# Performance work log

Hardware: AMD Instinct MI355X
Metric: run time of the kernel (lower is better)

The kernel has to match this reference:

```python
import jax, jax.numpy as jnp
import numpy as np

T, B, D_IN, D_HID, D_OUT = 4096, 64, 64, 512, 64


def setup_inputs() -> dict:
    key = jax.random.key(0)
    k0, k1, k2, k3, k4 = jax.random.split(key, 5)
    h = jax.random.normal(k0, (B, D_HID), dtype=jnp.float32)
    x = jax.random.normal(k1, (T, B, D_IN), dtype=jnp.float32)
    # stable_init: uniform in [0.999, 1.001]
    a = 0.999 + 0.002 * jax.random.uniform(k2, (D_HID,), dtype=jnp.float32)
    # glorot_normal: std = sqrt(2 / (fan_in + fan_out))
    b = jax.random.normal(k3, (D_IN, D_HID), dtype=jnp.float32) * jnp.sqrt(2.0 / (D_IN + D_HID)).astype(jnp.float32)
    c = jax.random.normal(k4, (D_HID, D_OUT), dtype=jnp.float32) * jnp.sqrt(2.0 / (D_HID + D_OUT)).astype(jnp.float32)
    return {"h": h, "x": x, "a": a, "b": b, "c": c}


def reference(h, x, a, b, c):
    """Diagonal linear RNN (RNNNode step) unrolled over time.

    Per step (faithful to the flax module):
        h = h * a + x_t @ b
        y_t = h @ c
    h: [B, D_HID], x: [T, B, D_IN]. Returns (h_final, y: [T, B, D_OUT]).
    """
    # Precompute the input projection for all steps (batched GEMM, outside the scan)
    xb = jnp.einsum('tbi,ih->tbh', x, b)  # [T, B, D_HID]

    def step(h_t, xb_t):
        h_t = h_t * a + xb_t
        return h_t, h_t

    h_final, hs = jax.lax.scan(step, h, xb)  # hs: [T, B, D_HID]
    y = jnp.einsum('tbh,ho->tbo', hs, c)  # [T, B, D_OUT]
    return h_final, y
```

## Files before the change

### kernel.cpp

```cpp
#include <hip/hip_runtime.h>
#include <stdint.h>

#define T_  4096
#define B_  64
#define DI_ 64
#define DH_ 512
#define DO_ 64
#define L_  64
#define C_  (T_ / L_)

typedef __attribute__((ext_vector_type(8))) short bf16x8;
typedef __attribute__((ext_vector_type(2))) float f32x2;
typedef __attribute__((ext_vector_type(4))) float f32x4;
typedef __attribute__((ext_vector_type(8))) float f32x8;
typedef __attribute__((ext_vector_type(2))) __bf16 bfv2;
typedef __attribute__((ext_vector_type(4))) __bf16 bfv4;
typedef __attribute__((ext_vector_type(8))) __bf16 bfv8;

union U8 { uint4 q; bf16x8 v; bfv8 b; };
union U2 { unsigned u; bfv2 b; };

__device__ inline unsigned short f2b_rne(float f) {
    unsigned u = __float_as_uint(f);
    return (unsigned short)((u + 0x7fffu + ((u >> 16) & 1u)) >> 16);
}

__device__ inline void trunc_split8(const float4 v0, const float4 v1, U8& hi, U8& lo) {
    const unsigned u0 = __float_as_uint(v0.x), u1 = __float_as_uint(v0.y),
                   u2 = __float_as_uint(v0.z), u3 = __float_as_uint(v0.w),
                   u4 = __float_as_uint(v1.x), u5 = __float_as_uint(v1.y),
                   u6 = __float_as_uint(v1.z), u7 = __float_as_uint(v1.w);
    hi.q.x = __builtin_amdgcn_perm(u1, u0, 0x07060302u);
    hi.q.y = __builtin_amdgcn_perm(u3, u2, 0x07060302u);
    hi.q.z = __builtin_amdgcn_perm(u5, u4, 0x07060302u);
    hi.q.w = __builtin_amdgcn_perm(u7, u6, 0x07060302u);
    const unsigned l0 = __float_as_uint(v0.x - __uint_as_float(u0 & 0xffff0000u));
    const unsigned l1 = __float_as_uint(v0.y - __uint_as_float(u1 & 0xffff0000u));
    const unsigned l2 = __float_as_uint(v0.z - __uint_as_float(u2 & 0xffff0000u));
    const unsigned l3 = __float_as_uint(v0.w - __uint_as_float(u3 & 0xffff0000u));
    const unsigned l4 = __float_as_uint(v1.x - __uint_as_float(u4 & 0xffff0000u));
    const unsigned l5 = __float_as_uint(v1.y - __uint_as_float(u5 & 0xffff0000u));
    const unsigned l6 = __float_as_uint(v1.z - __uint_as_float(u6 & 0xffff0000u));
    const unsigned l7 = __float_as_uint(v1.w - __uint_as_float(u7 & 0xffff0000u));
    lo.q.x = __builtin_amdgcn_perm(l1, l0, 0x07060302u);
    lo.q.y = __builtin_amdgcn_perm(l3, l2, 0x07060302u);
    lo.q.z = __builtin_amdgcn_perm(l5, l4, 0x07060302u);
    lo.q.w = __builtin_amdgcn_perm(l7, l6, 0x07060302u);
}

__global__ __launch_bounds__(256) void k_frags(
    const float* __restrict__ bmat, const float* __restrict__ cmat,
    const float* __restrict__ a,
    unsigned short* __restrict__ bhi, unsigned short* __restrict__ be1,
    unsigned short* __restrict__ be2,
    unsigned short* __restrict__ CwEh, unsigned short* __restrict__ CwEl,
    float* __restrict__ u_arr)
{
    const int t = blockIdx.x * 256 + threadIdx.x;
    if (t < 512) u_arr[t] = logf(a[t]);
    if (t < 32768) {
        const int j = t & 7, n = (t >> 3) & 15, g = (t >> 7) & 3;
        const int nt = (t >> 9) & 31, kb = (t >> 14) & 1;
        const int h = nt * 16 + n;
        const float v = bmat[(size_t)(kb * 32 + g * 8 + j) * DH_ + h];
        const float u = logf(a[h]);
        bhi[t] = f2b_rne(v);
        be1[t] = f2b_rne(v * u);
        be2[t] = f2b_rne(v * u * u * 0.5f);
    }
    {
        const int j = t & 7;
        const int lane = (t >> 3) & 63;
        const int rem = t >> 9;
        const int nt = rem % 12, kb = rem / 12;
        const int h = kb * 32 + (lane >> 4) * 8 + j;
        const int n = nt * 16 + (lane & 15);
        const int m = n >> 6, o = n & 63;
        const float av = a[h];
        const float u = logf(av);
        const float w = (m == 0) ? av : ((m == 1) ? av * u : av * u * u * 0.5f);
        const float v = w * cmat[(size_t)h * DO_ + o];
        unsigned short hi16 = (unsigned short)(__float_as_uint(v) >> 16);
        float lo = v - __uint_as_float(((unsigned)hi16) << 16);
        CwEh[t] = hi16;
        CwEl[t] = (unsigned short)(__float_as_uint(lo) >> 16);
    }
}

__global__ __launch_bounds__(256) void k_D(
    const float* __restrict__ bmat, const float* __restrict__ cmat,
    const float* __restrict__ u_arr, unsigned short* __restrict__ Dstk)
{
    const int mt   = blockIdx.x;
    const int tid  = threadIdx.x;
    const int lane = tid & 63;
    const int nt   = tid >> 6;
    const int lm   = lane & 15;
    const int lg   = lane >> 4;

    const int kposr = mt * 16 + lm;
    int p, i;
    if (kposr < 128) { i = kposr >> 1; p = kposr & 1; }
    else             { p = 2; i = kposr - 128; }

    f32x4 acc = {0.f, 0.f, 0.f, 0.f};
#pragma unroll
    for (int kb = 0; kb < 16; ++kb) {
        const int h0 = kb * 32 + lg * 8;
        const float4 b0 = *(const float4*)(bmat + (size_t)i * DH_ + h0);
        const float4 b1 = *(const float4*)(bmat + (size_t)i * DH_ + h0 + 4);
        const float4 w0 = *(const float4*)(u_arr + h0);
        const float4 w1 = *(const float4*)(u_arr + h0 + 4);
        const float bv[8] = {b0.x, b0.y, b0.z, b0.w, b1.x, b1.y, b1.z, b1.w};
        const float uv[8] = {w0.x, w0.y, w0.z, w0.w, w1.x, w1.y, w1.z, w1.w};
        U8 af, cf;
        bfv8 ab, cb;
#pragma unroll
        for (int j = 0; j < 8; ++j) {
            const float wp = (p == 0) ? 1.f : ((p == 1) ? uv[j] : uv[j] * uv[j] * 0.5f);
            ab[j] = (__bf16)(bv[j] * wp);
            cb[j] = (__bf16)cmat[(size_t)(h0 + j) * DO_ + nt * 16 + lm];
        }
        af.b = ab; cf.b = cb;
        acc = __builtin_amdgcn_mfma_f32_16x16x32_bf16(af.v, cf.v, acc, 0, 0, 0);
    }

#pragma unroll
    for (int rg = 0; rg < 4; ++rg) {
        const int kpos = mt * 16 + lg * 4 + rg;
        const int o    = nt * 16 + lm;
        Dstk[((size_t)((kpos >> 5) * 4 + (o >> 4)) * 64 + ((kpos >> 3) & 3) * 16 + (o & 15)) * 8 + (kpos & 7)]
            = f2b_rne(acc[rg]);
    }
}

__global__ __launch_bounds__(256) void k_mom(
    const float* __restrict__ x, unsigned short* __restrict__ Xm)
{
    const int c   = blockIdx.x;
    const int idx = blockIdx.y * 256 + threadIdx.x;
    const float* xp = x + (size_t)c * 64 * 4096 + idx;

    float m0 = 0.f, m1 = 0.f, m2 = 0.f;
#pragma unroll
    for (int s = 0; s < 64; ++s) {
        const float v = xp[(size_t)s * 4096];
        const float t = (float)(63 - s);
        m0 += v;
        m1 = fmaf(t, v, m1);
        m2 = fmaf(t * t, v, m2);
    }
    __bf16* Xb = (__bf16*)Xm;
    Xb[(size_t)(c * 3 + 0) * 4096 + idx] = (__bf16)m0;
    Xb[(size_t)(c * 3 + 1) * 4096 + idx] = (__bf16)m1;
    Xb[(size_t)(c * 3 + 2) * 4096 + idx] = (__bf16)m2;
}

__global__ __launch_bounds__(512) void k_rg(
    const unsigned short* __restrict__ Xm,
    const unsigned short* __restrict__ bhi, const unsigned short* __restrict__ be1,
    const unsigned short* __restrict__ be2,
    float* __restrict__ r)
{
    const int c    = blockIdx.x;
    const int nh   = blockIdx.y;
    const int tid  = threadIdx.x;
    const int lane = tid & 63;
    const int w    = tid >> 6;
    const int lm   = lane & 15;
    const int lg   = lane >> 4;

    bf16x8 af[4][6];
#pragma unroll
    for (int mt = 0; mt < 4; ++mt)
#pragma unroll
        for (int kb = 0; kb < 6; ++kb) {
            const int mom = kb >> 1;
            af[mt][kb] = *(const bf16x8*)(Xm + (size_t)(c * 3 + mom) * 4096
                                          + (mt * 16 + lm) * 64 + (kb & 1) * 32 + lg * 8);
        }

    bf16x8 bfr[6][2];
#pragma unroll
    for (int kb = 0; kb < 6; ++kb) {
        const int mom = kb >> 1;
        const unsigned short* base = (mom == 0) ? bhi : (mom == 1) ? be1 : be2;
#pragma unroll
        for (int nt = 0; nt < 2; ++nt) {
            const int ntg = nh * 16 + w * 2 + nt;
            bfr[kb][nt] = *(const bf16x8*)(base + ((size_t)((kb & 1) * 32 + ntg) * 64 + lane) * 8);
        }
    }

    f32x4 acc[4][2];
#pragma unroll
    for (int mt = 0; mt < 4; ++mt)
#pragma unroll
        for (int nt = 0; nt < 2; ++nt) acc[mt][nt] = (f32x4){0.f, 0.f, 0.f, 0.f};

#pragma unroll
    for (int kb = 0; kb < 6; ++kb)
#pragma unroll
        for (int nt = 0; nt < 2; ++nt)
#pragma unroll
            for (int mt = 0; mt < 4; ++mt)
                acc[mt][nt] = __builtin_amdgcn_mfma_f32_16x16x32_bf16(af[mt][kb], bfr[kb][nt], acc[mt][nt], 0, 0, 0);

#pragma unroll
    for (int mt = 0; mt < 4; ++mt)
#pragma unroll
        for (int nt = 0; nt < 2; ++nt)
#pragma unroll
            for (int rg = 0; rg < 4; ++rg) {
                const int bb = mt * 16 + lg * 4 + rg;
                const int h  = nh * 256 + w * 32 + nt * 16 + lm;
                r[((size_t)c * B_ + bb) * DH_ + h] = acc[mt][nt][rg];
            }
}

__global__ __launch_bounds__(512) void k_scan(
    const float* __restrict__ h0, const float* __restrict__ a,
    float* __restrict__ r, float* __restrict__ hfin)
{
    const int bb  = blockIdx.x;
    const int hid = threadIdx.x;
    const size_t base = (size_t)bb * DH_ + hid;

    float rv[C_];
#pragma unroll
    for (int c = 0; c < C_; ++c) rv[c] = r[(size_t)c * B_ * DH_ + base];

    float h  = h0[base];
    float aL = a[hid];
#pragma unroll
    for (int q = 0; q < 6; ++q) aL = aL * aL;

#pragma unroll
    for (int c = 0; c < C_; ++c) {
        r[(size_t)c * B_ * DH_ + base] = h;
        h = fmaf(h, aL, rv[c]);
    }
    hfin[base] = h;
}

__global__ __launch_bounds__(256) void k_E(
    const float* __restrict__ Hst,
    const unsigned short* __restrict__ CwEh, const unsigned short* __restrict__ CwEl,
    float* __restrict__ E)
{
    const int bx   = blockIdx.x;
    const int c    = bx >> 2;
    const int ms   = bx & 3;
    const int nb   = blockIdx.y;
    const int tid  = threadIdx.x;
    const int lane = tid & 63;
    const int w    = tid >> 6;
    const int lm   = lane & 15;
    const int lg   = lane >> 4;

    f32x4 acc = {0.f, 0.f, 0.f, 0.f};
    const int ntg = nb * 4 + w;

    for (int kb = 0; kb < 16; ++kb) {
        const float* ap = Hst + (size_t)(c * 64 + ms * 16 + lm) * DH_ + kb * 32 + lg * 8;
        U8 ahi, alo;
        trunc_split8(*(const float4*)ap, *(const float4*)(ap + 4), ahi, alo);
        const size_t fo = ((size_t)(kb * 12 + ntg) * 64 + lane) * 8;
        const bf16x8 bh = *(const bf16x8*)(CwEh + fo);
        const bf16x8 bl = *(const bf16x8*)(CwEl + fo);
        acc = __builtin_amdgcn_mfma_f32_16x16x32_bf16(ahi.v, bh, acc, 0, 0, 0);
        acc = __builtin_amdgcn_mfma_f32_16x16x32_bf16(alo.v, bh, acc, 0, 0, 0);
        acc = __builtin_amdgcn_mfma_f32_16x16x32_bf16(ahi.v, bl, acc, 0, 0, 0);
    }

#pragma unroll
    for (int rg = 0; rg < 4; ++rg) {
        const int row = ms * 16 + lg * 4 + rg;
        E[(size_t)(c * 64 + row) * 192 + ntg * 16 + lm] = acc[rg];
    }
}

__global__ __launch_bounds__(512, 8) void k_y(
    const float* __restrict__ x,
    const unsigned short* __restrict__ Dstk,
    const float* __restrict__ E,
    float* __restrict__ y)
{
    __shared__ __align__(16) unsigned short At[64 * 192];

    const int c    = blockIdx.x;
    const int bb   = blockIdx.y;
    const int tid  = threadIdx.x;
    const int lane = tid & 63;
    const int w    = tid >> 6;
    const int lm   = lane & 15;
    const int lg   = lane >> 4;
    const int mp   = w >> 2;
    const int oq   = w & 3;
    const int o    = oq * 16 + lm;

    if (tid < 64) {
        const int i = tid;
        const float* xp = x + ((size_t)(c * 64) * 64 + bb) * 64 + i;
        float S0 = 0.f, S1 = 0.f, S2 = 0.f;
        char* Ab = (char*)At;
#pragma unroll 8
        for (int s = 0; s < 64; ++s) {
            const float v = xp[(size_t)s * 4096];
            const float sf = (float)s;
            S0 += v;
            S1 = fmaf(sf, v, S1);
            S2 = fmaf(sf * sf, v, S2);
            const float A0 = S0;
            const float A1 = fmaf(sf, S0, -S1);
            const float A2 = fmaf(sf, fmaf(sf, S0, -2.0f * S1), S2);
            const int f = (s & 7) << 4;
            U2 pk; pk.b = __builtin_convertvector((f32x2){A0, A1}, bfv2);
            *(unsigned*)(Ab + ((s * 384 + 4 * i) ^ f)) = pk.u;
            *(__bf16*)(Ab + ((s * 384 + 256 + 2 * i) ^ f)) = (__bf16)A2;
        }
    }
    __syncthreads();

    const size_t erow = (size_t)(c * 64 + bb) * 192;
    const float e0 = E[erow + o];
    const float e1 = E[erow + 64 + o];
    const float e2 = E[erow + 128 + o];

    {
        const int row0 = (mp * 2 + 0) * 16 + lm;
        const int row1 = (mp * 2 + 1) * 16 + lm;
        const int f0 = (row0 & 7) << 4;
        const int f1 = (row1 & 7) << 4;
        const char* Ab = (const char*)At;

        f32x4 acc0 = {0.f, 0.f, 0.f, 0.f};
        f32x4 acc1 = {0.f, 0.f, 0.f, 0.f};

        __builtin_amdgcn_s_setprio(1);
#pragma unroll
        for (int kb = 0; kb < 6; ++kb) {
            const int b2k = kb * 64 + lg * 16;
            const bf16x8 a0 = *(const bf16x8*)(Ab + ((row0 * 384 + b2k) ^ f0));
            const bf16x8 a1 = *(const bf16x8*)(Ab + ((row1 * 384 + b2k) ^ f1));
            const bf16x8 df = *(const bf16x8*)(Dstk + ((size_t)(kb * 4 + oq) * 64 + lane) * 8);
            acc0 = __builtin_amdgcn_mfma_f32_16x16x32_bf16(a0, df, acc0, 0, 0, 0);
            acc1 = __builtin_amdgcn_mfma_f32_16x16x32_bf16(a1, df, acc1, 0, 0, 0);
        }
        __builtin_amdgcn_s_setprio(0);

#pragma unroll
        for (int rg = 0; rg < 4; ++rg) {
            const int sr0 = (mp * 2 + 0) * 16 + lg * 4 + rg;
            const int sr1 = (mp * 2 + 1) * 16 + lg * 4 + rg;
            const float s0f = (float)sr0, s1f = (float)sr1;
            const float y0 = acc0[rg] + fmaf(s0f, fmaf(s0f, e2, e1), e0);
            const float y1 = acc1[rg] + fmaf(s1f, fmaf(s1f, e2, e1), e0);
            y[(((size_t)(c * 64 + sr0)) * 64 + bb) * 64 + o] = y0;
            y[(((size_t)(c * 64 + sr1)) * 64 + bb) * 64 + o] = y1;
        }
    }
}

extern "C" void kernel_launch(void* const* d_in, const int* in_sizes, int n_in,
                              void* d_out, int out_size, void* d_ws, size_t ws_size,
                              hipStream_t stream) {
    (void)in_sizes; (void)n_in; (void)out_size; (void)ws_size;

    const float* h0 = (const float*)d_in[0];
    const float* x  = (const float*)d_in[1];
    const float* a  = (const float*)d_in[2];
    const float* bm = (const float*)d_in[3];
    const float* cm = (const float*)d_in[4];

    float* out  = (float*)d_out;
    float* hfin = out;
    float* y    = out + (size_t)B_ * DH_;

    float* r = (float*)d_ws;
    unsigned short* bhi  = (unsigned short*)(r + (size_t)C_ * B_ * DH_);
    unsigned short* be1  = bhi + 32768;
    unsigned short* be2  = be1 + 32768;
    unsigned short* CwEh = be2 + 32768;
    unsigned short* CwEl = CwEh + 98304;
    unsigned short* Dstk = CwEl + 98304;
    unsigned short* Xm   = Dstk + 12288;
    float* E = (float*)(Xm + (size_t)C_ * 3 * 4096);
    float* u_arr = E + (size_t)4096 * 192;

    k_frags<<<dim3(384), 256, 0, stream>>>(bm, cm, a, bhi, be1, be2, CwEh, CwEl, u_arr);
    k_D<<<dim3(12), 256, 0, stream>>>(bm, cm, u_arr, Dstk);
    k_mom<<<dim3(C_, 16), 256, 0, stream>>>(x, Xm);
    k_rg<<<dim3(C_, 2), 512, 0, stream>>>(Xm, bhi, be1, be2, r);
    k_scan<<<dim3(B_), 512, 0, stream>>>(h0, a, r, hfin);
    k_E<<<dim3(4 * C_, 3), 256, 0, stream>>>(r, CwEh, CwEl, E);
    k_y<<<dim3(C_, B_), 512, 0, stream>>>(x, Dstk, E, y);
}
```

Measured before the change: 108.1 us.

## Merge prep kernels into one launch and parallelize k_y prefix moments

Folds k_frags, k_D and k_mom into a single k_prep launch, dispatching on block index, and drops the u_arr buffer by recomputing logf(a) inside the D computation. This removes two kernel launches and the serial dependency through u_arr. In k_y, the 64-step serial prefix over time that ran on one wave is split across all 8 waves: each computes local moments for 8 steps, they exchange partials through shared memory, and then each finishes its own segment. The trade is an extra barrier and shared buffer, plus redundant logf calls.

```diff
diff --git a/kernel.cpp b/kernel.cpp
--- a/kernel.cpp
+++ b/kernel.cpp
@@ -14,7 +14,6 @@
 typedef __attribute__((ext_vector_type(4))) float f32x4;
 typedef __attribute__((ext_vector_type(8))) float f32x8;
 typedef __attribute__((ext_vector_type(2))) __bf16 bfv2;
-typedef __attribute__((ext_vector_type(4))) __bf16 bfv4;
 typedef __attribute__((ext_vector_type(8))) __bf16 bfv8;
 
 union U8 { uint4 q; bf16x8 v; bfv8 b; };
@@ -48,112 +47,106 @@
     lo.q.w = __builtin_amdgcn_perm(l7, l6, 0x07060302u);
 }
 
-__global__ __launch_bounds__(256) void k_frags(
+__global__ __launch_bounds__(256) void k_prep(
     const float* __restrict__ bmat, const float* __restrict__ cmat,
-    const float* __restrict__ a,
+    const float* __restrict__ a, const float* __restrict__ x,
     unsigned short* __restrict__ bhi, unsigned short* __restrict__ be1,
     unsigned short* __restrict__ be2,
     unsigned short* __restrict__ CwEh, unsigned short* __restrict__ CwEl,
-    float* __restrict__ u_arr)
+    unsigned short* __restrict__ Dstk, unsigned short* __restrict__ Xm)
 {
-    const int t = blockIdx.x * 256 + threadIdx.x;
-    if (t < 512) u_arr[t] = logf(a[t]);
-    if (t < 32768) {
-        const int j = t & 7, n = (t >> 3) & 15, g = (t >> 7) & 3;
-        const int nt = (t >> 9) & 31, kb = (t >> 14) & 1;
-        const int h = nt * 16 + n;
-        const float v = bmat[(size_t)(kb * 32 + g * 8 + j) * DH_ + h];
-        const float u = logf(a[h]);
-        bhi[t] = f2b_rne(v);
-        be1[t] = f2b_rne(v * u);
-        be2[t] = f2b_rne(v * u * u * 0.5f);
-    }
-    {
-        const int j = t & 7;
-        const int lane = (t >> 3) & 63;
-        const int rem = t >> 9;
-        const int nt = rem % 12, kb = rem / 12;
-        const int h = kb * 32 + (lane >> 4) * 8 + j;
-        const int n = nt * 16 + (lane & 15);
-        const int m = n >> 6, o = n & 63;
-        const float av = a[h];
-        const float u = logf(av);
-        const float w = (m == 0) ? av : ((m == 1) ? av * u : av * u * u * 0.5f);
-        const float v = w * cmat[(size_t)h * DO_ + o];
-        unsigned short hi16 = (unsigned short)(__float_as_uint(v) >> 16);
-        float lo = v - __uint_as_float(((unsigned)hi16) << 16);
-        CwEh[t] = hi16;
-        CwEl[t] = (unsigned short)(__float_as_uint(lo) >> 16);
-    }
-}
-
-__global__ __launch_bounds__(256) void k_D(
-    const float* __restrict__ bmat, const float* __restrict__ cmat,
-    const float* __restrict__ u_arr, unsigned short* __restrict__ Dstk)
-{
-    const int mt   = blockIdx.x;
-    const int tid  = threadIdx.x;
-    const int lane = tid & 63;
-    const int nt   = tid >> 6;
-    const int lm   = lane & 15;
-    const int lg   = lane >> 4;
-
-    const int kposr = mt * 16 + lm;
-    int p, i;
-    if (kposr < 128) { i = kposr >> 1; p = kposr & 1; }
-    else             { p = 2; i = kposr - 128; }
-
-    f32x4 acc = {0.f, 0.f, 0.f, 0.f};
-#pragma unroll
-    for (int kb = 0; kb < 16; ++kb) {
-        const int h0 = kb * 32 + lg * 8;
-        const float4 b0 = *(const float4*)(bmat + (size_t)i * DH_ + h0);
-        const float4 b1 = *(const float4*)(bmat + (size_t)i * DH_ + h0 + 4);
-        const float4 w0 = *(const float4*)(u_arr + h0);
-        const float4 w1 = *(const float4*)(u_arr + h0 + 4);
-        const float bv[8] = {b0.x, b0.y, b0.z, b0.w, b1.x, b1.y, b1.z, b1.w};
-        const float uv[8] = {w0.x, w0.y, w0.z, w0.w, w1.x, w1.y, w1.z, w1.w};
-        U8 af, cf;
-        bfv8 ab, cb;
-#pragma unroll
-        for (int j = 0; j < 8; ++j) {
-            const float wp = (p == 0) ? 1.f : ((p == 1) ? uv[j] : uv[j] * uv[j] * 0.5f);
-            ab[j] = (__bf16)(bv[j] * wp);
-            cb[j] = (__bf16)cmat[(size_t)(h0 + j) * DO_ + nt * 16 + lm];
-        }
-        af.b = ab; cf.b = cb;
-        acc = __builtin_amdgcn_mfma_f32_16x16x32_bf16(af.v, cf.v, acc, 0, 0, 0);
-    }
-
-#pragma unroll
-    for (int rg = 0; rg < 4; ++rg) {
-        const int kpos = mt * 16 + lg * 4 + rg;
-        const int o    = nt * 16 + lm;
-        Dstk[((size_t)((kpos >> 5) * 4 + (o >> 4)) * 64 + ((kpos >> 3) & 3) * 16 + (o & 15)) * 8 + (kpos & 7)]
-            = f2b_rne(acc[rg]);
-    }
-}
-
-__global__ __launch_bounds__(256) void k_mom(
-    const float* __restrict__ x, unsigned short* __restrict__ Xm)
-{
-    const int c   = blockIdx.x;
-    const int idx = blockIdx.y * 256 + threadIdx.x;
-    const float* xp = x + (size_t)c * 64 * 4096 + idx;
-
-    float m0 = 0.f, m1 = 0.f, m2 = 0.f;
-#pragma unroll
-    for (int s = 0; s < 64; ++s) {
-        const float v = xp[(size_t)s * 4096];
-        const float t = (float)(63 - s);
-        m0 += v;
-        m1 = fmaf(t, v, m1);
-        m2 = fmaf(t * t, v, m2);
-    }
-    __bf16* Xb = (__bf16*)Xm;
-    Xb[(size_t)(c * 3 + 0) * 4096 + idx] = (__bf16)m0;
-    Xb[(size_t)(c * 3 + 1) * 4096 + idx] = (__bf16)m1;
-    Xb[(size_t)(c * 3 + 2) * 4096 + idx] = (__bf16)m2;
+    const int bx = blockIdx.x;
+    if (bx < 384) {
+        const int t = bx * 256 + threadIdx.x;
+        if (t < 32768) {
+            const int j = t & 7, n = (t >> 3) & 15, g = (t >> 7) & 3;
+            const int nt = (t >> 9) & 31, kb = (t >> 14) & 1;
+            const int h = nt * 16 + n;
+            const float v = bmat[(size_t)(kb * 32 + g * 8 + j) * DH_ + h];
+            const float u = logf(a[h]);
+            bhi[t] = f2b_rne(v);
+            be1[t] = f2b_rne(v * u);
+            be2[t] = f2b_rne(v * u * u * 0.5f);
+        }
+        {
+            const int j = t & 7;
+            const int lane = (t >> 3) & 63;
+            const int rem = t >> 9;
+            const int nt = rem % 12, kb = rem / 12;
+            const int h = kb * 32 + (lane >> 4) * 8 + j;
+            const int n = nt * 16 + (lane & 15);
+            const int m = n >> 6, o = n & 63;
+            const float av = a[h];
+            const float u = logf(av);
+            const float w = (m == 0) ? av : ((m == 1) ? av * u : av * u * u * 0.5f);
+            const float v = w * cmat[(size_t)h * DO_ + o];
+            unsigned short hi16 = (unsigned short)(__float_as_uint(v) >> 16);
+            float lo = v - __uint_as_float(((unsigned)hi16) << 16);
+            CwEh[t] = hi16;
+            CwEl[t] = (unsigned short)(__float_as_uint(lo) >> 16);
+        }
+    } else if (bx < 396) {
+        const int mt   = bx - 384;
+        const int tid  = threadIdx.x;
+        const int lane = tid & 63;
+        const int nt   = tid >> 6;
+        const int lm   = lane & 15;
+        const int lg   = lane >> 4;
+
+        const int kposr = mt * 16 + lm;
+        int p, i;
+        if (kposr < 128) { i = kposr >> 1; p = kposr & 1; }
+        else             { p = 2; i = kposr - 128; }
+
+        f32x4 acc = {0.f, 0.f, 0.f, 0.f};
+#pragma unroll
+        for (int kb = 0; kb < 16; ++kb) {
+            const int h0 = kb * 32 + lg * 8;
+            const float4 b0 = *(const float4*)(bmat + (size_t)i * DH_ + h0);
+            const float4 b1 = *(const float4*)(bmat + (size_t)i * DH_ + h0 + 4);
+            const float bv[8] = {b0.x, b0.y, b0.z, b0.w, b1.x, b1.y, b1.z, b1.w};
+            U8 af, cf;
+            bfv8 ab, cb;
+#pragma unroll
+            for (int j = 0; j < 8; ++j) {
+                float wp = 1.f;
+                if (p > 0) {
+                    const float u = logf(a[h0 + j]);
+                    wp = (p == 1) ? u : u * u * 0.5f;
+                }
+                ab[j] = (__bf16)(bv[j] * wp);
+                cb[j] = (__bf16)cmat[(size_t)(h0 + j) * DO_ + nt * 16 + lm];
+            }
+            af.b = ab; cf.b = cb;
+            acc = __builtin_amdgcn_mfma_f32_16x16x32_bf16(af.v, cf.v, acc, 0, 0, 0);
+        }
+#pragma unroll
+        for (int rg = 0; rg < 4; ++rg) {
+            const int kpos = mt * 16 + lg * 4 + rg;
+            const int o    = nt * 16 + lm;
+            Dstk[((size_t)((kpos >> 5) * 4 + (o >> 4)) * 64 + ((kpos >> 3) & 3) * 16 + (o & 15)) * 8 + (kpos & 7)]
+                = f2b_rne(acc[rg]);
+        }
+    } else {
+        const int m   = bx - 396;
+        const int c   = m >> 4;
+        const int idx = (m & 15) * 256 + threadIdx.x;
+        const float* xp = x + (size_t)c * 64 * 4096 + idx;
+
+        float m0 = 0.f, m1 = 0.f, m2 = 0.f;
+#pragma unroll
+        for (int s = 0; s < 64; ++s) {
+            const float v = xp[(size_t)s * 4096];
+            const float t = (float)(63 - s);
+            m0 += v;
+            m1 = fmaf(t, v, m1);
+            m2 = fmaf(t * t, v, m2);
+        }
+        __bf16* Xb = (__bf16*)Xm;
+        Xb[(size_t)(c * 3 + 0) * 4096 + idx] = (__bf16)m0;
+        Xb[(size_t)(c * 3 + 1) * 4096 + idx] = (__bf16)m1;
+        Xb[(size_t)(c * 3 + 2) * 4096 + idx] = (__bf16)m2;
+    }
 }
 
 __global__ __launch_bounds__(512) void k_rg(
@@ -287,6 +280,7 @@
     float* __restrict__ y)
 {
     __shared__ __align__(16) unsigned short At[64 * 192];
+    __shared__ float Lb[3][8][64];
 
     const int c    = blockIdx.x;
     const int bb   = blockIdx.y;
@@ -299,22 +293,45 @@
     const int oq   = w & 3;
     const int o    = oq * 16 + lm;
 
-    if (tid < 64) {
-        const int i = tid;
-        const float* xp = x + ((size_t)(c * 64) * 64 + bb) * 64 + i;
+    {
+        const int i = tid & 63;
+        const int j = w;
+
+        const float* xp = x + (((size_t)(c * 64 + j * 8)) * 64 + bb) * 64 + i;
+        float v[8];
+#pragma unroll
+        for (int t = 0; t < 8; ++t) v[t] = xp[(size_t)t * 4096];
+
+        float L0 = 0.f, L1 = 0.f, L2 = 0.f;
+#pragma unroll
+        for (int t = 0; t < 8; ++t) {
+            const float sf = (float)(j * 8 + t);
+            L0 += v[t];
+            L1 = fmaf(sf, v[t], L1);
+            L2 = fmaf(sf * sf, v[t], L2);
+        }
+        Lb[0][j][i] = L0; Lb[1][j][i] = L1; Lb[2][j][i] = L2;
+        __syncthreads();
+
         float S0 = 0.f, S1 = 0.f, S2 = 0.f;
+        for (int k = 0; k < j; ++k) {
+            S0 += Lb[0][k][i];
+            S1 += Lb[1][k][i];
+            S2 += Lb[2][k][i];
+        }
+
         char* Ab = (char*)At;
-#pragma unroll 8
-        for (int s = 0; s < 64; ++s) {
-            const float v = xp[(size_t)s * 4096];
+#pragma unroll
+        for (int t = 0; t < 8; ++t) {
+            const int s = j * 8 + t;
             const float sf = (float)s;
-            S0 += v;
-            S1 = fmaf(sf, v, S1);
-            S2 = fmaf(sf * sf, v, S2);
+            S0 += v[t];
+            S1 = fmaf(sf, v[t], S1);
+            S2 = fmaf(sf * sf, v[t], S2);
             const float A0 = S0;
             const float A1 = fmaf(sf, S0, -S1);
             const float A2 = fmaf(sf, fmaf(sf, S0, -2.0f * S1), S2);
-            const int f = (s & 7) << 4;
+            const int f = t << 4;
             U2 pk; pk.b = __builtin_convertvector((f32x2){A0, A1}, bfv2);
             *(unsigned*)(Ab + ((s * 384 + 4 * i) ^ f)) = pk.u;
             *(__bf16*)(Ab + ((s * 384 + 256 + 2 * i) ^ f)) = (__bf16)A2;
@@ -386,11 +403,8 @@
     unsigned short* Dstk = CwEl + 98304;
     unsigned short* Xm   = Dstk + 12288;
     float* E = (float*)(Xm + (size_t)C_ * 3 * 4096);
-    float* u_arr = E + (size_t)4096 * 192;
-
-    k_frags<<<dim3(384), 256, 0, stream>>>(bm, cm, a, bhi, be1, be2, CwEh, CwEl, u_arr);
-    k_D<<<dim3(12), 256, 0, stream>>>(bm, cm, u_arr, Dstk);
-    k_mom<<<dim3(C_, 16), 256, 0, stream>>>(x, Xm);
+
+    k_prep<<<dim3(1420), 256, 0, stream>>>(bm, cm, a, x, bhi, be1, be2, CwEh, CwEl, Dstk, Xm);
     k_rg<<<dim3(C_, 2), 512, 0, stream>>>(Xm, bhi, be1, be2, r);
     k_scan<<<dim3(B_), 512, 0, stream>>>(h0, a, r, hfin);
     k_E<<<dim3(4 * C_, 3), 256, 0, stream>>>(r, CwEh, CwEl, E);
```

Result: slower. 124.1 us (+14.8%).
